# Kernel tuning notes

Hardware: AMD Instinct MI355X
Metric: run time of the kernel (lower is better)

Reference implementation:

```python
import jax, jax.numpy as jnp
import numpy as np

N = 50000
IN_DIM, HID, OUT = 128, 64, 128
HEADS = 4
EPS_LN = 1e-5
NEG_SLOPE = 0.2


def gat_conv(x, W, a_src, a_dst, bias, src, dst, concat):
    """PyG-style GATConv. x:[N,F], W:[F,H*C], a_src/a_dst:[H,C], src/dst:[E]."""
    H, C = a_src.shape
    h = (x @ W).reshape(-1, H, C)                 # [N,H,C]
    e_src = jnp.sum(h * a_src, axis=-1)           # [N,H]
    e_dst = jnp.sum(h * a_dst, axis=-1)           # [N,H]
    e = jax.nn.leaky_relu(e_src[src] + e_dst[dst], NEG_SLOPE)  # [E,H]
    # softmax over incoming edges per destination node (numerically stable)
    m = jax.ops.segment_max(e, dst, num_segments=N)            # [N,H]
    m = jnp.where(jnp.isfinite(m), m, 0.0)
    ex = jnp.exp(e - m[dst])                                   # [E,H]
    denom = jax.ops.segment_sum(ex, dst, num_segments=N)       # [N,H]
    alpha = ex / (denom[dst] + 1e-16)                          # [E,H]
    msg = h[src] * alpha[:, :, None]                           # [E,H,C]
    out = jax.ops.segment_sum(msg, dst, num_segments=N)        # [N,H,C]
    out = out.reshape(-1, H * C) if concat else out.mean(axis=1)
    return out + bias


def layer_norm(x, gamma, beta):
    mu = jnp.mean(x, axis=-1, keepdims=True)
    var = jnp.mean(jnp.square(x - mu), axis=-1, keepdims=True)
    return (x - mu) * jax.lax.rsqrt(var + EPS_LN) * gamma + beta


def setup_inputs() -> dict:
    key = jax.random.key(0)
    ks = jax.random.split(key, 12)
    x = jax.random.normal(ks[0], (N, IN_DIM), dtype=jnp.float32)
    edge_index = jax.random.randint(ks[1], (2, 800000), 0, N, dtype=jnp.int64)
    s1 = 1.0 / np.sqrt(IN_DIM)
    W1 = jax.random.normal(ks[2], (IN_DIM, HEADS * HID), dtype=jnp.float32) * s1
    a_src1 = jax.random.normal(ks[3], (HEADS, HID), dtype=jnp.float32) * 0.1
    a_dst1 = jax.random.normal(ks[4], (HEADS, HID), dtype=jnp.float32) * 0.1
    b1 = jnp.zeros((HEADS * HID,), dtype=jnp.float32)
    s2 = 1.0 / np.sqrt(HEADS * HID)
    W2 = jax.random.normal(ks[5], (HEADS * HID, HEADS * OUT), dtype=jnp.float32) * s2
    a_src2 = jax.random.normal(ks[6], (HEADS, OUT), dtype=jnp.float32) * 0.1
    a_dst2 = jax.random.normal(ks[7], (HEADS, OUT), dtype=jnp.float32) * 0.1
    b2 = jnp.zeros((OUT,), dtype=jnp.float32)
    gamma = jnp.ones((OUT,), dtype=jnp.float32)
    beta = jnp.zeros((OUT,), dtype=jnp.float32)
    return {"x": x, "edge_index": edge_index, "W1": W1, "a_src1": a_src1,
            "a_dst1": a_dst1, "b1": b1, "W2": W2, "a_src2": a_src2,
            "a_dst2": a_dst2, "b2": b2, "gamma": gamma, "beta": beta}


def reference(x, edge_index, W1, a_src1, a_dst1, b1, W2, a_src2, a_dst2, b2, gamma, beta):
    # PyG GATConv adds self loops by default
    loop = jnp.arange(N, dtype=edge_index.dtype)
    src = jnp.concatenate([edge_index[0], loop])
    dst = jnp.concatenate([edge_index[1], loop])
    h = gat_conv(x, W1, a_src1, a_dst1, b1, src, dst, concat=True)   # [N, 256]
    h = jax.nn.relu(h)
    h = gat_conv(h, W2, a_src2, a_dst2, b2, src, dst, concat=False)  # [N, 128]
    return layer_norm(h, gamma, beta)
```

## Files before the change

### kernel.cpp

```cpp
#include <hip/hip_runtime.h>
#include <hip/hip_fp16.h>
#include <cstdint>
#include <cstddef>


constexpr int NNODES = 50000;
constexpr int NBINS = (NNODES + 255) >> 8;
constexpr int ABLOCKS = 256;

typedef unsigned short bf16_t;
typedef __attribute__((ext_vector_type(8))) short bf16x8;
typedef __attribute__((ext_vector_type(4))) float f32x4;

__device__ __forceinline__ float bf2f(bf16_t b) {
  return __uint_as_float(((unsigned int)b) << 16);
}
__device__ __forceinline__ bf16_t f2bf(float f) {
  unsigned int u = __float_as_uint(f);
  u += 0x7fffu + ((u >> 16) & 1u);
  return (bf16_t)(u >> 16);
}
__device__ __forceinline__ float4 bf4_to_f4(ushort4 v) {
  return make_float4(bf2f(v.x), bf2f(v.y), bf2f(v.z), bf2f(v.w));
}
__device__ __forceinline__ ushort4 f4_to_bf4(float4 v) {
  return make_ushort4(f2bf(v.x), f2bf(v.y), f2bf(v.z), f2bf(v.w));
}
__device__ __forceinline__ ushort f2h(float f) {
  __half h = __float2half_rn(f);
  return *(ushort*)&h;
}
__device__ __forceinline__ float h2f(ushort u) {
  __half h; *(ushort*)&h = u;
  return __half2float(h);
}
__device__ __forceinline__ float lrelu(float x) { return x > 0.f ? x : 0.2f * x; }
__device__ __forceinline__ int clampi(int v, int lo, int hi) {
  return v < lo ? lo : (v > hi ? hi : v);
}
__device__ __forceinline__ int load_edge(const void* ei, int mode, int idx) {
  if (mode) return (int)((const long long*)ei)[idx];
  return ((const int*)ei)[idx];
}

__device__ __forceinline__ int block_detect_mode(const int* ei32, int* nz_sm) {
  if (threadIdx.x == 0) *nz_sm = 0;
  __syncthreads();
  if (threadIdx.x < 256 && ei32[2 * threadIdx.x + 1] != 0) atomicAdd(nz_sm, 1);
  __syncthreads();
  return (*nz_sm == 0) ? 1 : 0;
}


__global__ void convert_x_kernel(const float* __restrict__ x, bf16_t* __restrict__ xb,
                                 int n4) {
  int i = blockIdx.x * blockDim.x + threadIdx.x;
  if (i >= n4) return;
  float4 v = *(const float4*)(x + 4 * (size_t)i);
  *(ushort4*)(xb + 4 * (size_t)i) = f4_to_bf4(v);
}

template <int K, int NC>
__global__ void transpose_w_kernel(const float* __restrict__ W, bf16_t* __restrict__ Wt) {
  int n = blockIdx.x;
  int k = threadIdx.x;
  Wt[(size_t)n * K + k] = f2bf(W[(size_t)k * NC + n]);
}

__global__ void proj2_kernel(const float* __restrict__ W2,
                             const float* __restrict__ asrc2,
                             const float* __restrict__ adst2,
                             float* __restrict__ ws2, float* __restrict__ wd2) {
  int h = blockIdx.x;
  int k = threadIdx.x;
  const float* wrow = W2 + (size_t)k * 512 + h * 128;
  const float* as = asrc2 + h * 128;
  const float* ad = adst2 + h * 128;
  float s = 0.f, d = 0.f;
  for (int c = 0; c < 128; ++c) { s += wrow[c] * as[c]; d += wrow[c] * ad[c]; }
  ws2[h * 256 + k] = s;
  wd2[h * 256 + k] = d;
}

__global__ __launch_bounds__(1024) void wstack_kernel(const float* __restrict__ W2,
                                                      bf16_t* __restrict__ Wt2s) {
  int c = blockIdx.x;
  int t = threadIdx.x;
  int h = t >> 8, k = t & 255;
  Wt2s[(size_t)c * 1024 + t] = f2bf(W2[(size_t)k * 512 + h * 128 + c] * 0.25f);
}

__global__ __launch_bounds__(256) void binhist_kernel(
    const void* __restrict__ ei, int* __restrict__ blockBin,
    int e0, int et, int chunk) {
  __shared__ int h[NBINS];
  __shared__ int nzsm;
  int mode = block_detect_mode((const int*)ei, &nzsm);
  int t = threadIdx.x, blk = blockIdx.x;
  for (int i = t; i < NBINS; i += 256) h[i] = 0;
  __syncthreads();
  int lo = blk * chunk, hi = min(et, lo + chunk);
  for (int e = lo + t; e < hi; e += 256) {
    int dst = (e < e0) ? load_edge(ei, mode, e0 + e) : (e - e0);
    dst = clampi(dst, 0, NNODES - 1);
    atomicAdd(&h[dst >> 8], 1);
  }
  __syncthreads();
  for (int i = t; i < NBINS; i += 256) blockBin[i * ABLOCKS + blk] = h[i];
}

__global__ __launch_bounds__(ABLOCKS) void binscanA_kernel(int* __restrict__ blockBin,
                                                           int* __restrict__ binTotal) {
  __shared__ int sm[ABLOCKS];
  int b = blockIdx.x, t = threadIdx.x;
  int orig = blockBin[b * ABLOCKS + t];
  sm[t] = orig;
  __syncthreads();
  for (int off = 1; off < ABLOCKS; off <<= 1) {
    int u = (t >= off) ? sm[t - off] : 0;
    __syncthreads();
    sm[t] += u;
    __syncthreads();
  }
  blockBin[b * ABLOCKS + t] = sm[t] - orig;
  if (t == ABLOCKS - 1) binTotal[b] = sm[ABLOCKS - 1];
}

__global__ __launch_bounds__(256) void binscanB_kernel(const int* __restrict__ binTotal,
                                                       int* __restrict__ binStart) {
  __shared__ int sm[256];
  int t = threadIdx.x;
  int orig = (t < NBINS) ? binTotal[t] : 0;
  sm[t] = orig;
  __syncthreads();
  for (int off = 1; off < 256; off <<= 1) {
    int u = (t >= off) ? sm[t - off] : 0;
    __syncthreads();
    sm[t] += u;
    __syncthreads();
  }
  if (t < NBINS) binStart[t] = sm[t] - orig;
  if (t == 255) binStart[NBINS] = sm[255];
}

__global__ __launch_bounds__(256) void binscatter_kernel(
    const void* __restrict__ ei, const int* __restrict__ blockBin,
    const int* __restrict__ binStart, int2* __restrict__ pairs,
    int e0, int et, int chunk) {
  __shared__ int cur[NBINS];
  __shared__ int nzsm;
  int mode = block_detect_mode((const int*)ei, &nzsm);
  int t = threadIdx.x, blk = blockIdx.x;
  for (int i = t; i < NBINS; i += 256)
    cur[i] = binStart[i] + blockBin[i * ABLOCKS + blk];
  __syncthreads();
  int lo = blk * chunk, hi = min(et, lo + chunk);
  for (int e = lo + t; e < hi; e += 256) {
    int src, dst;
    if (e < e0) { src = load_edge(ei, mode, e); dst = load_edge(ei, mode, e0 + e); }
    else        { src = dst = e - e0; }
    src = clampi(src, 0, NNODES - 1);
    dst = clampi(dst, 0, NNODES - 1);
    int p = atomicAdd(&cur[dst >> 8], 1);
    pairs[p] = make_int2(src, dst);
  }
}

__global__ __launch_bounds__(256) void csrbin_kernel(const int2* __restrict__ pairs,
                                                     const int* __restrict__ binStart,
                                                     int* __restrict__ rowptr,
                                                     int* __restrict__ col) {
  __shared__ int cnt[256];
  __shared__ int sc[256];
  int b = blockIdx.x, t = threadIdx.x;
  int node0 = b << 8;
  int es = binStart[b], ee = binStart[b + 1];
  cnt[t] = 0;
  __syncthreads();
  for (int p = es + t; p < ee; p += 256) {
    int2 pr = pairs[p];
    int d = clampi(pr.y - node0, 0, 255);
    atomicAdd(&cnt[d], 1);
  }
  __syncthreads();
  int orig = cnt[t];
  sc[t] = orig;
  __syncthreads();
  for (int off = 1; off < 256; off <<= 1) {
    int u = (t >= off) ? sc[t - off] : 0;
    __syncthreads();
    sc[t] += u;
    __syncthreads();
  }
  int excl = sc[t] - orig;
  if (node0 + t < NNODES) rowptr[node0 + t] = es + excl;
  if (b == NBINS - 1 && t == 0) rowptr[NNODES] = ee;
  cnt[t] = excl;
  __syncthreads();
  for (int p = es + t; p < ee; p += 256) {
    int2 pr = pairs[p];
    int d = clampi(pr.y - node0, 0, 255);
    int pos = atomicAdd(&cnt[d], 1);
    col[es + pos] = pr.x;
  }
}

__global__ __launch_bounds__(256) void gemm1s_kernel(
    const bf16_t* __restrict__ A, const bf16_t* __restrict__ Wt,
    bf16_t* __restrict__ C, const float* __restrict__ asrc,
    const float* __restrict__ adst, float* __restrict__ es,
    float* __restrict__ ed, int M) {
  __shared__ __align__(16) ushort As[64 * 40];
  __shared__ __align__(16) ushort Bs[64 * 40];
  const int t    = threadIdx.x;
  const int wv   = t >> 6;
  const int lane = t & 63;
  const int m    = lane & 15;
  const int quad = lane >> 4;
  const int bm = blockIdx.x * 64, bn = blockIdx.y * 64;
  const int srow = t & 63;
  const int sk8  = t >> 6;

  f32x4 acc0 = {0.f, 0.f, 0.f, 0.f};
  f32x4 acc1 = {0.f, 0.f, 0.f, 0.f};
  f32x4 acc2 = {0.f, 0.f, 0.f, 0.f};
  f32x4 acc3 = {0.f, 0.f, 0.f, 0.f};

  for (int k0 = 0; k0 < 128; k0 += 32) {
    int ga = clampi(bm + srow, 0, M - 1);
    float4 av = *(const float4*)(A + (size_t)ga * 128 + k0 + sk8 * 8);
    *(float4*)(&As[srow * 40 + sk8 * 8]) = av;
    float4 bv = *(const float4*)(Wt + (size_t)(bn + srow) * 128 + k0 + sk8 * 8);
    *(float4*)(&Bs[srow * 40 + sk8 * 8]) = bv;
    __syncthreads();

    bf16x8 af = *(const bf16x8*)(&As[(wv * 16 + m) * 40 + quad * 8]);
    bf16x8 b0 = *(const bf16x8*)(&Bs[(0 * 16 + m) * 40 + quad * 8]);
    bf16x8 b1 = *(const bf16x8*)(&Bs[(1 * 16 + m) * 40 + quad * 8]);
    bf16x8 b2 = *(const bf16x8*)(&Bs[(2 * 16 + m) * 40 + quad * 8]);
    bf16x8 b3 = *(const bf16x8*)(&Bs[(3 * 16 + m) * 40 + quad * 8]);
    acc0 = __builtin_amdgcn_mfma_f32_16x16x32_bf16(af, b0, acc0, 0, 0, 0);
    acc1 = __builtin_amdgcn_mfma_f32_16x16x32_bf16(af, b1, acc1, 0, 0, 0);
    acc2 = __builtin_amdgcn_mfma_f32_16x16x32_bf16(af, b2, acc2, 0, 0, 0);
    acc3 = __builtin_amdgcn_mfma_f32_16x16x32_bf16(af, b3, acc3, 0, 0, 0);
    __syncthreads();
  }

  float as0 = asrc[bn +  0 + m], as1 = asrc[bn + 16 + m];
  float as2 = asrc[bn + 32 + m], as3 = asrc[bn + 48 + m];
  float ad0 = adst[bn +  0 + m], ad1 = adst[bn + 16 + m];
  float ad2 = adst[bn + 32 + m], ad3 = adst[bn + 48 + m];
  const int hd = bn >> 6;

#pragma unroll
  for (int r = 0; r < 4; ++r) {
    int row = bm + wv * 16 + quad * 4 + r;
    float ps = acc0[r] * as0 + acc1[r] * as1 + acc2[r] * as2 + acc3[r] * as3;
    float pd = acc0[r] * ad0 + acc1[r] * ad1 + acc2[r] * ad2 + acc3[r] * ad3;
    for (int mm = 1; mm < 16; mm <<= 1) {
      ps += __shfl_xor(ps, mm);
      pd += __shfl_xor(pd, mm);
    }
    if (row < M) {
      size_t base = (size_t)row * 256 + bn;
      C[base +  0 + m] = f2bf(acc0[r]);
      C[base + 16 + m] = f2bf(acc1[r]);
      C[base + 32 + m] = f2bf(acc2[r]);
      C[base + 48 + m] = f2bf(acc3[r]);
      if (m == 0) {
        es[row * 4 + hd] = ps;
        ed[row * 4 + hd] = pd;
      }
    }
  }
}

__global__ __launch_bounds__(256) void alpha_kernel(
    const float* __restrict__ es, const float* __restrict__ ed,
    const int* __restrict__ rowptr, const int* __restrict__ col,
    ushort* __restrict__ alpha) {
  int node = (blockIdx.x * blockDim.x + threadIdx.x) >> 4;
  if (node >= NNODES) return;
  int l16 = threadIdx.x & 15;
  int beg = rowptr[node], end = rowptr[node + 1];
  float4 edv = *(const float4*)(ed + node * 4);
  float4 l = make_float4(0.f, 0.f, 0.f, 0.f);
  for (int p = beg + l16; p < end; p += 16) {
    int s = col[p];
    float4 e = *(const float4*)(es + s * 4);
    l.x += __expf(lrelu(e.x + edv.x));
    l.y += __expf(lrelu(e.y + edv.y));
    l.z += __expf(lrelu(e.z + edv.z));
    l.w += __expf(lrelu(e.w + edv.w));
  }
  for (int off = 1; off < 16; off <<= 1) {
    l.x += __shfl_xor(l.x, off);
    l.y += __shfl_xor(l.y, off);
    l.z += __shfl_xor(l.z, off);
    l.w += __shfl_xor(l.w, off);
  }
  float4 il = make_float4(1.f / (l.x + 1e-16f), 1.f / (l.y + 1e-16f),
                          1.f / (l.z + 1e-16f), 1.f / (l.w + 1e-16f));
  for (int p = beg + l16; p < end; p += 16) {
    int s = col[p];
    float4 e = *(const float4*)(es + s * 4);
    ushort4 a;
    a.x = f2h(__expf(lrelu(e.x + edv.x)) * il.x);
    a.y = f2h(__expf(lrelu(e.y + edv.y)) * il.y);
    a.z = f2h(__expf(lrelu(e.z + edv.z)) * il.z);
    a.w = f2h(__expf(lrelu(e.w + edv.w)) * il.w);
    *(ushort4*)(alpha + (size_t)p * 4) = a;
  }
}

__global__ __launch_bounds__(256) void aggregate1_kernel(
    const bf16_t* __restrict__ h, const ushort* __restrict__ alpha,
    const int* __restrict__ rowptr, const int* __restrict__ col,
    const float* __restrict__ b1, bf16_t* __restrict__ out,
    const float* __restrict__ ws2, const float* __restrict__ wd2,
    float* __restrict__ es2, float* __restrict__ ed2) {
  int node = (blockIdx.x * blockDim.x + threadIdx.x) >> 6;
  if (node >= NNODES) return;
  int lane = threadIdx.x & 63;
  int head = lane >> 4;
  int beg = rowptr[node], end = rowptr[node + 1];
  const ushort4* hb = (const ushort4*)h;
  float4 acc = make_float4(0.f, 0.f, 0.f, 0.f);
  int j = beg;
  for (; j + 4 <= end; j += 4) {
    int s0 = col[j], s1 = col[j + 1], s2 = col[j + 2], s3 = col[j + 3];
    ushort u0 = alpha[(size_t)(j + 0) * 4 + head];
    ushort u1 = alpha[(size_t)(j + 1) * 4 + head];
    ushort u2 = alpha[(size_t)(j + 2) * 4 + head];
    ushort u3 = alpha[(size_t)(j + 3) * 4 + head];
    ushort4 r0 = hb[(size_t)s0 * 64 + lane];
    ushort4 r1 = hb[(size_t)s1 * 64 + lane];
    ushort4 r2 = hb[(size_t)s2 * 64 + lane];
    ushort4 r3 = hb[(size_t)s3 * 64 + lane];
    float a0 = h2f(u0), a1 = h2f(u1), a2 = h2f(u2), a3 = h2f(u3);
    float4 v0 = bf4_to_f4(r0), v1 = bf4_to_f4(r1);
    float4 v2 = bf4_to_f4(r2), v3 = bf4_to_f4(r3);
    acc.x += a0 * v0.x + a1 * v1.x + a2 * v2.x + a3 * v3.x;
    acc.y += a0 * v0.y + a1 * v1.y + a2 * v2.y + a3 * v3.y;
    acc.z += a0 * v0.z + a1 * v1.z + a2 * v2.z + a3 * v3.z;
    acc.w += a0 * v0.w + a1 * v1.w + a2 * v2.w + a3 * v3.w;
  }
  for (; j < end; ++j) {
    int s0 = col[j];
    float a0 = h2f(alpha[(size_t)j * 4 + head]);
    float4 v0 = bf4_to_f4(hb[(size_t)s0 * 64 + lane]);
    acc.x += a0 * v0.x;
    acc.y += a0 * v0.y;
    acc.z += a0 * v0.z;
    acc.w += a0 * v0.w;
  }
  float4 bb = *(const float4*)(b1 + 4 * lane);
  float4 o;
  o.x = fmaxf(acc.x + bb.x, 0.f);
  o.y = fmaxf(acc.y + bb.y, 0.f);
  o.z = fmaxf(acc.z + bb.z, 0.f);
  o.w = fmaxf(acc.w + bb.w, 0.f);
  *(ushort4*)(out + (size_t)node * 256 + 4 * lane) = f4_to_bf4(o);

  float s2[4], d2[4];
#pragma unroll
  for (int hh = 0; hh < 4; ++hh) {
    float4 wv = *(const float4*)(ws2 + hh * 256 + 4 * lane);
    float4 dv = *(const float4*)(wd2 + hh * 256 + 4 * lane);
    s2[hh] = o.x * wv.x + o.y * wv.y + o.z * wv.z + o.w * wv.w;
    d2[hh] = o.x * dv.x + o.y * dv.y + o.z * dv.z + o.w * dv.w;
  }
  for (int mm = 1; mm < 64; mm <<= 1) {
#pragma unroll
    for (int hh = 0; hh < 4; ++hh) {
      s2[hh] += __shfl_xor(s2[hh], mm);
      d2[hh] += __shfl_xor(d2[hh], mm);
    }
  }
  if (lane == 0) {
#pragma unroll
    for (int hh = 0; hh < 4; ++hh) {
      es2[node * 4 + hh] = s2[hh];
      ed2[node * 4 + hh] = d2[hh];
    }
  }
}

__device__ __forceinline__ void fma4h(float (&acc)[4][4], ushort4 q, float4 v) {
  float f0 = h2f(q.x), f1 = h2f(q.y), f2 = h2f(q.z), f3 = h2f(q.w);
  acc[0][0] += f0 * v.x; acc[0][1] += f0 * v.y; acc[0][2] += f0 * v.z; acc[0][3] += f0 * v.w;
  acc[1][0] += f1 * v.x; acc[1][1] += f1 * v.y; acc[1][2] += f1 * v.z; acc[1][3] += f1 * v.w;
  acc[2][0] += f2 * v.x; acc[2][1] += f2 * v.y; acc[2][2] += f2 * v.z; acc[2][3] += f2 * v.w;
  acc[3][0] += f3 * v.x; acc[3][1] += f3 * v.y; acc[3][2] += f3 * v.z; acc[3][3] += f3 * v.w;
}

__global__ __launch_bounds__(256) void agg2in_kernel(
    const bf16_t* __restrict__ out1, const ushort* __restrict__ alpha,
    const int* __restrict__ rowptr, const int* __restrict__ col,
    bf16_t* __restrict__ z, int n0, int n1) {
  int node = n0 + ((blockIdx.x * blockDim.x + threadIdx.x) >> 6);
  if (node >= n1) return;
  int lane = threadIdx.x & 63;
  int beg = rowptr[node], end = rowptr[node + 1];
  const ushort4* hb = (const ushort4*)out1;
  float acc[4][4] = {{0.f,0.f,0.f,0.f},{0.f,0.f,0.f,0.f},
                     {0.f,0.f,0.f,0.f},{0.f,0.f,0.f,0.f}};
  int j = beg;
  for (; j + 4 <= end; j += 4) {
    int s0 = col[j], s1 = col[j + 1], s2 = col[j + 2], s3 = col[j + 3];
    ushort4 q0 = *(const ushort4*)(alpha + (size_t)(j + 0) * 4);
    ushort4 q1 = *(const ushort4*)(alpha + (size_t)(j + 1) * 4);
    ushort4 q2 = *(const ushort4*)(alpha + (size_t)(j + 2) * 4);
    ushort4 q3 = *(const ushort4*)(alpha + (size_t)(j + 3) * 4);
    ushort4 r0 = hb[(size_t)s0 * 64 + lane];
    ushort4 r1 = hb[(size_t)s1 * 64 + lane];
    ushort4 r2 = hb[(size_t)s2 * 64 + lane];
    ushort4 r3 = hb[(size_t)s3 * 64 + lane];
    fma4h(acc, q0, bf4_to_f4(r0));
    fma4h(acc, q1, bf4_to_f4(r1));
    fma4h(acc, q2, bf4_to_f4(r2));
    fma4h(acc, q3, bf4_to_f4(r3));
  }
  for (; j < end; ++j) {
    int s0 = col[j];
    ushort4 q0 = *(const ushort4*)(alpha + (size_t)j * 4);
    ushort4 r0 = hb[(size_t)s0 * 64 + lane];
    fma4h(acc, q0, bf4_to_f4(r0));
  }
  bf16_t* zr = z + (size_t)(node - n0) * 1024 + 4 * lane;
#pragma unroll
  for (int h = 0; h < 4; ++h) {
    *(ushort4*)(zr + h * 256) =
        f4_to_bf4(make_float4(acc[h][0], acc[h][1], acc[h][2], acc[h][3]));
  }
}

__global__ __launch_bounds__(256) void gemm2ln_kernel(
    const bf16_t* __restrict__ Z, const bf16_t* __restrict__ Wt2s,
    const float* __restrict__ b2, const float* __restrict__ gamma,
    const float* __restrict__ beta, float* __restrict__ out, int n0, int M) {
  __shared__ __align__(16) ushort As[64 * 40];
  __shared__ __align__(16) ushort Bs[128 * 40];
  const int t    = threadIdx.x;
  const int wv   = t >> 6;
  const int lane = t & 63;
  const int m    = lane & 15;
  const int quad = lane >> 4;
  const int bm   = blockIdx.x * 64;

  f32x4 c0 = {0.f,0.f,0.f,0.f}, c1 = c0, c2 = c0, c3 = c0;
  f32x4 c4 = c0, c5 = c0, c6 = c0, c7 = c0;

  const int arow = t & 63, ak8 = t >> 6;
  for (int k0 = 0; k0 < 1024; k0 += 32) {
    int ga = clampi(bm + arow, 0, M - 1);
    *(float4*)(&As[arow * 40 + ak8 * 8]) =
        *(const float4*)(Z + (size_t)ga * 1024 + k0 + ak8 * 8);
    {
      int q = t;
      *(float4*)(&Bs[(q >> 2) * 40 + (q & 3) * 8]) =
          *(const float4*)(Wt2s + (size_t)(q >> 2) * 1024 + k0 + (q & 3) * 8);
      q = t + 256;
      *(float4*)(&Bs[(q >> 2) * 40 + (q & 3) * 8]) =
          *(const float4*)(Wt2s + (size_t)(q >> 2) * 1024 + k0 + (q & 3) * 8);
    }
    __syncthreads();

    bf16x8 af = *(const bf16x8*)(&As[(wv * 16 + m) * 40 + quad * 8]);
    bf16x8 b0 = *(const bf16x8*)(&Bs[(0 * 16 + m) * 40 + quad * 8]);
    bf16x8 b1 = *(const bf16x8*)(&Bs[(1 * 16 + m) * 40 + quad * 8]);
    bf16x8 b2f = *(const bf16x8*)(&Bs[(2 * 16 + m) * 40 + quad * 8]);
    bf16x8 b3 = *(const bf16x8*)(&Bs[(3 * 16 + m) * 40 + quad * 8]);
    bf16x8 b4 = *(const bf16x8*)(&Bs[(4 * 16 + m) * 40 + quad * 8]);
    bf16x8 b5 = *(const bf16x8*)(&Bs[(5 * 16 + m) * 40 + quad * 8]);
    bf16x8 b6 = *(const bf16x8*)(&Bs[(6 * 16 + m) * 40 + quad * 8]);
    bf16x8 b7 = *(const bf16x8*)(&Bs[(7 * 16 + m) * 40 + quad * 8]);
    c0 = __builtin_amdgcn_mfma_f32_16x16x32_bf16(af, b0, c0, 0, 0, 0);
    c1 = __builtin_amdgcn_mfma_f32_16x16x32_bf16(af, b1, c1, 0, 0, 0);
    c2 = __builtin_amdgcn_mfma_f32_16x16x32_bf16(af, b2f, c2, 0, 0, 0);
    c3 = __builtin_amdgcn_mfma_f32_16x16x32_bf16(af, b3, c3, 0, 0, 0);
    c4 = __builtin_amdgcn_mfma_f32_16x16x32_bf16(af, b4, c4, 0, 0, 0);
    c5 = __builtin_amdgcn_mfma_f32_16x16x32_bf16(af, b5, c5, 0, 0, 0);
    c6 = __builtin_amdgcn_mfma_f32_16x16x32_bf16(af, b6, c6, 0, 0, 0);
    c7 = __builtin_amdgcn_mfma_f32_16x16x32_bf16(af, b7, c7, 0, 0, 0);
    __syncthreads();
  }

  float b2v[8], gv[8], btv[8];
#pragma unroll
  for (int n = 0; n < 8; ++n) {
    int c = n * 16 + m;
    b2v[n] = b2[c]; gv[n] = gamma[c]; btv[n] = beta[c];
  }
#pragma unroll
  for (int r = 0; r < 4; ++r) {
    float v0 = c0[r] + b2v[0], v1 = c1[r] + b2v[1];
    float v2 = c2[r] + b2v[2], v3 = c3[r] + b2v[3];
    float v4 = c4[r] + b2v[4], v5 = c5[r] + b2v[5];
    float v6 = c6[r] + b2v[6], v7 = c7[r] + b2v[7];
    float tsum = v0 + v1 + v2 + v3 + v4 + v5 + v6 + v7;
    tsum += __shfl_xor(tsum, 1); tsum += __shfl_xor(tsum, 2);
    tsum += __shfl_xor(tsum, 4); tsum += __shfl_xor(tsum, 8);
    float mu = tsum * (1.f / 128.f);
    float d0 = v0 - mu, d1 = v1 - mu, d2 = v2 - mu, d3 = v3 - mu;
    float d4 = v4 - mu, d5 = v5 - mu, d6 = v6 - mu, d7 = v7 - mu;
    float vq = d0*d0 + d1*d1 + d2*d2 + d3*d3 + d4*d4 + d5*d5 + d6*d6 + d7*d7;
    vq += __shfl_xor(vq, 1); vq += __shfl_xor(vq, 2);
    vq += __shfl_xor(vq, 4); vq += __shfl_xor(vq, 8);
    float rinv = rsqrtf(vq * (1.f / 128.f) + 1e-5f);
    int row = bm + wv * 16 + quad * 4 + r;
    if (row < M) {
      float* orow = out + (size_t)(n0 + row) * 128;
      orow[0 * 16 + m] = d0 * rinv * gv[0] + btv[0];
      orow[1 * 16 + m] = d1 * rinv * gv[1] + btv[1];
      orow[2 * 16 + m] = d2 * rinv * gv[2] + btv[2];
      orow[3 * 16 + m] = d3 * rinv * gv[3] + btv[3];
      orow[4 * 16 + m] = d4 * rinv * gv[4] + btv[4];
      orow[5 * 16 + m] = d5 * rinv * gv[5] + btv[5];
      orow[6 * 16 + m] = d6 * rinv * gv[6] + btv[6];
      orow[7 * 16 + m] = d7 * rinv * gv[7] + btv[7];
    }
  }
}


extern "C" void kernel_launch(void* const* d_in, const int* in_sizes, int n_in,
                              void* d_out, int out_size, void* d_ws, size_t ws_size,
                              hipStream_t stream) {
  const float* x     = (const float*)d_in[0];
  const void*  ei    = d_in[1];
  const float* W1    = (const float*)d_in[2];
  const float* asrc1 = (const float*)d_in[3];
  const float* adst1 = (const float*)d_in[4];
  const float* b1    = (const float*)d_in[5];
  const float* W2    = (const float*)d_in[6];
  const float* asrc2 = (const float*)d_in[7];
  const float* adst2 = (const float*)d_in[8];
  const float* b2    = (const float*)d_in[9];
  const float* gamma = (const float*)d_in[10];
  const float* beta  = (const float*)d_in[11];
  float* out = (float*)d_out;

  const int E0 = in_sizes[1] / 2;
  const int ET = E0 + NNODES;

  char* w = (char*)d_ws;
  bf16_t* z      = (bf16_t*)(w + 0);
  int2*   pairs  = (int2*)(w + 25600000);
  bf16_t* h1     = (bf16_t*)(w + 25600000);
  bf16_t* xb     = (bf16_t*)(w + 51200000);
  bf16_t* out1   = (bf16_t*)(w + 51200000);
  ushort* alpha  = (ushort*)(w + 76800000);
  float* es    = (float*)(w + 83600000);
  float* ed    = (float*)(w + 84400000);
  bf16_t* Wt1    = (bf16_t*)(w + 85200000);
  bf16_t* Wt2s   = (bf16_t*)(w + 85300000);
  float* ws2   = (float*)(w + 85564000);
  float* wd2   = (float*)(w + 85570000);
  int* rowptr   = (int*)(w + 85600000);
  int* binStart = (int*)(w + 85800064);
  int* binTotal = (int*)(w + 85801000);
  int* blockBin = (int*)(w + 85802000);
  int* col      = (int*)(w + 86200192);

  convert_x_kernel<<<(NNODES * 128 / 4 + 255) / 256, 256, 0, stream>>>(x, xb,
                                                                       NNODES * 128 / 4);
  transpose_w_kernel<128, 256><<<256, 128, 0, stream>>>(W1, Wt1);
  proj2_kernel<<<4, 256, 0, stream>>>(W2, asrc2, adst2, ws2, wd2);
  wstack_kernel<<<128, 1024, 0, stream>>>(W2, Wt2s);

  const int CHUNK = (ET + ABLOCKS - 1) / ABLOCKS;
  binhist_kernel<<<ABLOCKS, 256, 0, stream>>>(ei, blockBin, E0, ET, CHUNK);
  binscanA_kernel<<<NBINS, ABLOCKS, 0, stream>>>(blockBin, binTotal);
  binscanB_kernel<<<1, 256, 0, stream>>>(binTotal, binStart);
  binscatter_kernel<<<ABLOCKS, 256, 0, stream>>>(ei, blockBin, binStart, pairs,
                                                 E0, ET, CHUNK);
  csrbin_kernel<<<NBINS, 256, 0, stream>>>(pairs, binStart, rowptr, col);

  const int MB = (NNODES + 63) / 64;
  const int NODE_BLOCKS = (NNODES + 3) / 4;
  const int NODE_BLOCKS16 = (NNODES * 16 + 255) / 256;

  gemm1s_kernel<<<dim3(MB, 4), 256, 0, stream>>>(xb, Wt1, h1, asrc1, adst1,
                                                 es, ed, NNODES);
  alpha_kernel<<<NODE_BLOCKS16, 256, 0, stream>>>(es, ed, rowptr, col, alpha);
  aggregate1_kernel<<<NODE_BLOCKS, 256, 0, stream>>>(h1, alpha, rowptr, col, b1,
                                                     out1, ws2, wd2, es, ed);

  alpha_kernel<<<NODE_BLOCKS16, 256, 0, stream>>>(es, ed, rowptr, col, alpha);

  const int HALF = NNODES / 2;
  const int AB = (HALF * 64 + 255) / 256;
  const int GB = (HALF + 63) / 64;
  agg2in_kernel<<<AB, 256, 0, stream>>>(out1, alpha, rowptr, col, z, 0, HALF);
  gemm2ln_kernel<<<GB, 256, 0, stream>>>(z, Wt2s, b2, gamma, beta, out, 0, HALF);
  agg2in_kernel<<<AB, 256, 0, stream>>>(out1, alpha, rowptr, col, z, HALF, NNODES);
  gemm2ln_kernel<<<GB, 256, 0, stream>>>(z, Wt2s, b2, gamma, beta, out, HALF, HALF);
}
```

Measured before the change: 390.1 us.

## Quantize node features to int8 with per-row scales folded into attention weights

The layer-1 projected features and the layer-1 outputs are now stored as int8, with a per-node-per-head scale (layer 1) or per-node scale (layer 2). Each scale is folded into the fp16 alpha coefficients computed in alpha_kernel. This halves the bytes gathered per edge in the two aggregation kernels, which are bound by random-gather bandwidth. The cost is lost precision from 8-bit quantization, which risks accuracy tolerance failures, plus a small amount of extra max-reduction and scale traffic.

```diff
diff --git a/kernel.cpp b/kernel.cpp
--- a/kernel.cpp
+++ b/kernel.cpp
@@ -41,6 +41,9 @@
 __device__ __forceinline__ int load_edge(const void* ei, int mode, int idx) {
   if (mode) return (int)((const long long*)ei)[idx];
   return ((const int*)ei)[idx];
+}
+__device__ __forceinline__ float4 c4_to_f4(char4 v) {
+  return make_float4((float)v.x, (float)v.y, (float)v.z, (float)v.w);
 }
 
 __device__ __forceinline__ int block_detect_mode(const int* ei32, int* nz_sm) {
@@ -207,9 +210,9 @@
 
 __global__ __launch_bounds__(256) void gemm1s_kernel(
     const bf16_t* __restrict__ A, const bf16_t* __restrict__ Wt,
-    bf16_t* __restrict__ C, const float* __restrict__ asrc,
-    const float* __restrict__ adst, float* __restrict__ es,
-    float* __restrict__ ed, int M) {
+    char* __restrict__ h1q, float* __restrict__ scl1,
+    const float* __restrict__ asrc, const float* __restrict__ adst,
+    float* __restrict__ es, float* __restrict__ ed, int M) {
   __shared__ __align__(16) ushort As[64 * 40];
   __shared__ __align__(16) ushort Bs[64 * 40];
   const int t    = threadIdx.x;
@@ -257,17 +260,22 @@
     int row = bm + wv * 16 + quad * 4 + r;
     float ps = acc0[r] * as0 + acc1[r] * as1 + acc2[r] * as2 + acc3[r] * as3;
     float pd = acc0[r] * ad0 + acc1[r] * ad1 + acc2[r] * ad2 + acc3[r] * ad3;
+    float mx = fmaxf(fmaxf(fabsf(acc0[r]), fabsf(acc1[r])),
+                     fmaxf(fabsf(acc2[r]), fabsf(acc3[r])));
     for (int mm = 1; mm < 16; mm <<= 1) {
       ps += __shfl_xor(ps, mm);
       pd += __shfl_xor(pd, mm);
+      mx = fmaxf(mx, __shfl_xor(mx, mm));
     }
+    float inv = mx > 0.f ? 127.f / mx : 0.f;
     if (row < M) {
       size_t base = (size_t)row * 256 + bn;
-      C[base +  0 + m] = f2bf(acc0[r]);
-      C[base + 16 + m] = f2bf(acc1[r]);
-      C[base + 32 + m] = f2bf(acc2[r]);
-      C[base + 48 + m] = f2bf(acc3[r]);
+      h1q[base +  0 + m] = (char)__float2int_rn(acc0[r] * inv);
+      h1q[base + 16 + m] = (char)__float2int_rn(acc1[r] * inv);
+      h1q[base + 32 + m] = (char)__float2int_rn(acc2[r] * inv);
+      h1q[base + 48 + m] = (char)__float2int_rn(acc3[r] * inv);
       if (m == 0) {
+        scl1[row * 4 + hd] = mx * (1.f / 127.f);
         es[row * 4 + hd] = ps;
         ed[row * 4 + hd] = pd;
       }
@@ -275,10 +283,11 @@
   }
 }
 
+template <int SMODE>
 __global__ __launch_bounds__(256) void alpha_kernel(
     const float* __restrict__ es, const float* __restrict__ ed,
     const int* __restrict__ rowptr, const int* __restrict__ col,
-    ushort* __restrict__ alpha) {
+    const float* __restrict__ scales, ushort* __restrict__ alpha) {
   int node = (blockIdx.x * blockDim.x + threadIdx.x) >> 4;
   if (node >= NNODES) return;
   int l16 = threadIdx.x & 15;
@@ -304,19 +313,28 @@
   for (int p = beg + l16; p < end; p += 16) {
     int s = col[p];
     float4 e = *(const float4*)(es + s * 4);
+    float sx, sy, sz, sw;
+    if (SMODE == 0) {
+      float4 sc = *(const float4*)(scales + s * 4);
+      sx = sc.x; sy = sc.y; sz = sc.z; sw = sc.w;
+    } else {
+      float sc = scales[s];
+      sx = sc; sy = sc; sz = sc; sw = sc;
+    }
     ushort4 a;
-    a.x = f2h(__expf(lrelu(e.x + edv.x)) * il.x);
-    a.y = f2h(__expf(lrelu(e.y + edv.y)) * il.y);
-    a.z = f2h(__expf(lrelu(e.z + edv.z)) * il.z);
-    a.w = f2h(__expf(lrelu(e.w + edv.w)) * il.w);
+    a.x = f2h(__expf(lrelu(e.x + edv.x)) * il.x * sx);
+    a.y = f2h(__expf(lrelu(e.y + edv.y)) * il.y * sy);
+    a.z = f2h(__expf(lrelu(e.z + edv.z)) * il.z * sz);
+    a.w = f2h(__expf(lrelu(e.w + edv.w)) * il.w * sw);
     *(ushort4*)(alpha + (size_t)p * 4) = a;
   }
 }
 
 __global__ __launch_bounds__(256) void aggregate1_kernel(
-    const bf16_t* __restrict__ h, const ushort* __restrict__ alpha,
+    const char* __restrict__ h1q, const ushort* __restrict__ alpha,
     const int* __restrict__ rowptr, const int* __restrict__ col,
-    const float* __restrict__ b1, bf16_t* __restrict__ out,
+    const float* __restrict__ b1, char* __restrict__ out1q,
+    float* __restrict__ scl2,
     const float* __restrict__ ws2, const float* __restrict__ wd2,
     float* __restrict__ es2, float* __restrict__ ed2) {
   int node = (blockIdx.x * blockDim.x + threadIdx.x) >> 6;
@@ -324,7 +342,6 @@
   int lane = threadIdx.x & 63;
   int head = lane >> 4;
   int beg = rowptr[node], end = rowptr[node + 1];
-  const ushort4* hb = (const ushort4*)h;
   float4 acc = make_float4(0.f, 0.f, 0.f, 0.f);
   int j = beg;
   for (; j + 4 <= end; j += 4) {
@@ -333,13 +350,13 @@
     ushort u1 = alpha[(size_t)(j + 1) * 4 + head];
     ushort u2 = alpha[(size_t)(j + 2) * 4 + head];
     ushort u3 = alpha[(size_t)(j + 3) * 4 + head];
-    ushort4 r0 = hb[(size_t)s0 * 64 + lane];
-    ushort4 r1 = hb[(size_t)s1 * 64 + lane];
-    ushort4 r2 = hb[(size_t)s2 * 64 + lane];
-    ushort4 r3 = hb[(size_t)s3 * 64 + lane];
+    char4 r0 = *(const char4*)(h1q + (size_t)s0 * 256 + 4 * lane);
+    char4 r1 = *(const char4*)(h1q + (size_t)s1 * 256 + 4 * lane);
+    char4 r2 = *(const char4*)(h1q + (size_t)s2 * 256 + 4 * lane);
+    char4 r3 = *(const char4*)(h1q + (size_t)s3 * 256 + 4 * lane);
     float a0 = h2f(u0), a1 = h2f(u1), a2 = h2f(u2), a3 = h2f(u3);
-    float4 v0 = bf4_to_f4(r0), v1 = bf4_to_f4(r1);
-    float4 v2 = bf4_to_f4(r2), v3 = bf4_to_f4(r3);
+    float4 v0 = c4_to_f4(r0), v1 = c4_to_f4(r1);
+    float4 v2 = c4_to_f4(r2), v3 = c4_to_f4(r3);
     acc.x += a0 * v0.x + a1 * v1.x + a2 * v2.x + a3 * v3.x;
     acc.y += a0 * v0.y + a1 * v1.y + a2 * v2.y + a3 * v3.y;
     acc.z += a0 * v0.z + a1 * v1.z + a2 * v2.z + a3 * v3.z;
@@ -348,7 +365,7 @@
   for (; j < end; ++j) {
     int s0 = col[j];
     float a0 = h2f(alpha[(size_t)j * 4 + head]);
-    float4 v0 = bf4_to_f4(hb[(size_t)s0 * 64 + lane]);
+    float4 v0 = c4_to_f4(*(const char4*)(h1q + (size_t)s0 * 256 + 4 * lane));
     acc.x += a0 * v0.x;
     acc.y += a0 * v0.y;
     acc.z += a0 * v0.z;
@@ -360,7 +377,6 @@
   o.y = fmaxf(acc.y + bb.y, 0.f);
   o.z = fmaxf(acc.z + bb.z, 0.f);
   o.w = fmaxf(acc.w + bb.w, 0.f);
-  *(ushort4*)(out + (size_t)node * 256 + 4 * lane) = f4_to_bf4(o);
 
   float s2[4], d2[4];
 #pragma unroll
@@ -377,7 +393,18 @@
       d2[hh] += __shfl_xor(d2[hh], mm);
     }
   }
+
+  float mx = fmaxf(fmaxf(o.x, o.y), fmaxf(o.z, o.w));
+  for (int mm = 1; mm < 64; mm <<= 1) mx = fmaxf(mx, __shfl_xor(mx, mm));
+  float inv = mx > 0.f ? 127.f / mx : 0.f;
+  char4 oq;
+  oq.x = (char)__float2int_rn(o.x * inv);
+  oq.y = (char)__float2int_rn(o.y * inv);
+  oq.z = (char)__float2int_rn(o.z * inv);
+  oq.w = (char)__float2int_rn(o.w * inv);
+  *(char4*)(out1q + (size_t)node * 256 + 4 * lane) = oq;
   if (lane == 0) {
+    scl2[node] = mx * (1.f / 127.f);
 #pragma unroll
     for (int hh = 0; hh < 4; ++hh) {
       es2[node * 4 + hh] = s2[hh];
@@ -395,14 +422,13 @@
 }
 
 __global__ __launch_bounds__(256) void agg2in_kernel(
-    const bf16_t* __restrict__ out1, const ushort* __restrict__ alpha,
+    const char* __restrict__ out1q, const ushort* __restrict__ alpha,
     const int* __restrict__ rowptr, const int* __restrict__ col,
     bf16_t* __restrict__ z, int n0, int n1) {
   int node = n0 + ((blockIdx.x * blockDim.x + threadIdx.x) >> 6);
   if (node >= n1) return;
   int lane = threadIdx.x & 63;
   int beg = rowptr[node], end = rowptr[node + 1];
-  const ushort4* hb = (const ushort4*)out1;
   float acc[4][4] = {{0.f,0.f,0.f,0.f},{0.f,0.f,0.f,0.f},
                      {0.f,0.f,0.f,0.f},{0.f,0.f,0.f,0.f}};
   int j = beg;
@@ -412,20 +438,20 @@
     ushort4 q1 = *(const ushort4*)(alpha + (size_t)(j + 1) * 4);
     ushort4 q2 = *(const ushort4*)(alpha + (size_t)(j + 2) * 4);
     ushort4 q3 = *(const ushort4*)(alpha + (size_t)(j + 3) * 4);
-    ushort4 r0 = hb[(size_t)s0 * 64 + lane];
-    ushort4 r1 = hb[(size_t)s1 * 64 + lane];
-    ushort4 r2 = hb[(size_t)s2 * 64 + lane];
-    ushort4 r3 = hb[(size_t)s3 * 64 + lane];
-    fma4h(acc, q0, bf4_to_f4(r0));
-    fma4h(acc, q1, bf4_to_f4(r1));
-    fma4h(acc, q2, bf4_to_f4(r2));
-    fma4h(acc, q3, bf4_to_f4(r3));
+    char4 r0 = *(const char4*)(out1q + (size_t)s0 * 256 + 4 * lane);
+    char4 r1 = *(const char4*)(out1q + (size_t)s1 * 256 + 4 * lane);
+    char4 r2 = *(const char4*)(out1q + (size_t)s2 * 256 + 4 * lane);
+    char4 r3 = *(const char4*)(out1q + (size_t)s3 * 256 + 4 * lane);
+    fma4h(acc, q0, c4_to_f4(r0));
+    fma4h(acc, q1, c4_to_f4(r1));
+    fma4h(acc, q2, c4_to_f4(r2));
+    fma4h(acc, q3, c4_to_f4(r3));
   }
   for (; j < end; ++j) {
     int s0 = col[j];
     ushort4 q0 = *(const ushort4*)(alpha + (size_t)j * 4);
-    ushort4 r0 = hb[(size_t)s0 * 64 + lane];
-    fma4h(acc, q0, bf4_to_f4(r0));
+    char4 r0 = *(const char4*)(out1q + (size_t)s0 * 256 + 4 * lane);
+    fma4h(acc, q0, c4_to_f4(r0));
   }
   bf16_t* zr = z + (size_t)(node - n0) * 1024 + 4 * lane;
 #pragma unroll
@@ -547,9 +573,11 @@
   char* w = (char*)d_ws;
   bf16_t* z      = (bf16_t*)(w + 0);
   int2*   pairs  = (int2*)(w + 25600000);
-  bf16_t* h1     = (bf16_t*)(w + 25600000);
+  char*   h1q    = (char*)(w + 25600000);
+  float*  scl1   = (float*)(w + 38400000);
   bf16_t* xb     = (bf16_t*)(w + 51200000);
-  bf16_t* out1   = (bf16_t*)(w + 51200000);
+  char*   out1q  = (char*)(w + 51200000);
+  float*  scl2   = (float*)(w + 64100000);
   ushort* alpha  = (ushort*)(w + 76800000);
   float* es    = (float*)(w + 83600000);
   float* ed    = (float*)(w + 84400000);
@@ -581,19 +609,21 @@
   const int NODE_BLOCKS = (NNODES + 3) / 4;
   const int NODE_BLOCKS16 = (NNODES * 16 + 255) / 256;
 
-  gemm1s_kernel<<<dim3(MB, 4), 256, 0, stream>>>(xb, Wt1, h1, asrc1, adst1,
-                                                 es, ed, NNODES);
-  alpha_kernel<<<NODE_BLOCKS16, 256, 0, stream>>>(es, ed, rowptr, col, alpha);
-  aggregate1_kernel<<<NODE_BLOCKS, 256, 0, stream>>>(h1, alpha, rowptr, col, b1,
-                                                     out1, ws2, wd2, es, ed);
-
-  alpha_kernel<<<NODE_BLOCKS16, 256, 0, stream>>>(es, ed, rowptr, col, alpha);
+  gemm1s_kernel<<<dim3(MB, 4), 256, 0, stream>>>(xb, Wt1, h1q, scl1,
+                                                 asrc1, adst1, es, ed, NNODES);
+  alpha_kernel<0><<<NODE_BLOCKS16, 256, 0, stream>>>(es, ed, rowptr, col,
+                                                     scl1, alpha);
+  aggregate1_kernel<<<NODE_BLOCKS, 256, 0, stream>>>(h1q, alpha, rowptr, col, b1,
+                                                     out1q, scl2, ws2, wd2, es, ed);
+
+  alpha_kernel<1><<<NODE_BLOCKS16, 256, 0, stream>>>(es, ed, rowptr, col,
+                                                     scl2, alpha);
 
   const int HALF = NNODES / 2;
   const int AB = (HALF * 64 + 255) / 256;
   const int GB = (HALF + 63) / 64;
-  agg2in_kernel<<<AB, 256, 0, stream>>>(out1, alpha, rowptr, col, z, 0, HALF);
+  agg2in_kernel<<<AB, 256, 0, stream>>>(out1q, alpha, rowptr, col, z, 0, HALF);
   gemm2ln_kernel<<<GB, 256, 0, stream>>>(z, Wt2s, b2, gamma, beta, out, 0, HALF);
-  agg2in_kernel<<<AB, 256, 0, stream>>>(out1, alpha, rowptr, col, z, HALF, NNODES);
+  agg2in_kernel<<<AB, 256, 0, stream>>>(out1q, alpha, rowptr, col, z, HALF, NNODES);
   gemm2ln_kernel<<<GB, 256, 0, stream>>>(z, Wt2s, b2, gamma, beta, out, HALF, HALF);
 }
```

Result: faster. 362.9 us (-7.0%).
